# Kernel tuning notes

Hardware: AMD Instinct MI355X
Metric: run time of the kernel (lower is better)

The kernel has to match this reference:

```python
import jax, jax.numpy as jnp
import numpy as np

N_NODES = 20000   # N
N_EDGES = 320000  # E (avg degree 16)
T_STEPS = 16      # T
IN_FEATS = 1      # F
HG = 64           # hidden_g
HT = 128          # hidden_t
LN_EPS = 1e-5


def _layer_norm(x, g, b):
    mu = jnp.mean(x, axis=-1, keepdims=True)
    var = jnp.mean((x - mu) ** 2, axis=-1, keepdims=True)
    return (x - mu) * jax.lax.rsqrt(var + LN_EPS) * g + b


def setup_inputs() -> dict:
    key = jax.random.key(0)
    k = jax.random.split(key, 16)
    r = lambda i, shape, s: jax.random.normal(k[i], shape, jnp.float32) * s
    return dict(
        x_seq=jax.random.normal(k[0], (1, T_STEPS, N_NODES, IN_FEATS), jnp.float32),
        edge_index=jax.random.randint(k[1], (2, N_EDGES), 0, N_NODES, dtype=jnp.int32),
        # SAGEConv layer 0: lin_l (aggregated neighbors, has bias) + lin_r (root)
        W_l0=r(2, (IN_FEATS, HG), 0.5), W_r0=r(3, (IN_FEATS, HG), 0.5), b0=jnp.zeros((HG,), jnp.float32),
        ln0_g=jnp.ones((HG,), jnp.float32), ln0_b=jnp.zeros((HG,), jnp.float32),
        # SAGEConv layer 1
        W_l1=r(4, (HG, HG), 0.1), W_r1=r(5, (HG, HG), 0.1), b1=jnp.zeros((HG,), jnp.float32),
        ln1_g=jnp.ones((HG,), jnp.float32), ln1_b=jnp.zeros((HG,), jnp.float32),
        # GRU (torch layout: gates r,z,n stacked along first dim)
        gru_Wih=r(6, (3 * HT, HG), 0.05), gru_Whh=r(7, (3 * HT, HT), 0.05),
        gru_bih=jnp.zeros((3 * HT,), jnp.float32), gru_bhh=jnp.zeros((3 * HT,), jnp.float32),
        # head
        head_W=r(8, (HT, 1), 0.05), head_b=jnp.zeros((1,), jnp.float32),
    )


def reference(x_seq, edge_index, W_l0, W_r0, b0, ln0_g, ln0_b,
              W_l1, W_r1, b1, ln1_g, ln1_b,
              gru_Wih, gru_Whh, gru_bih, gru_bhh, head_W, head_b):
    src, dst = edge_index[0], edge_index[1]
    # in-degree for mean aggregation (clamped to 1, like PyG mean aggr on isolated nodes)
    deg = jnp.clip(jax.ops.segment_sum(jnp.ones((N_EDGES,), jnp.float32), dst,
                                       num_segments=N_NODES), 1.0)[:, None]

    def sage(x, Wl, Wr, b):
        # mean over incoming neighbors, then lin_l(aggr) + lin_r(root)
        agg = jax.ops.segment_sum(x[src], dst, num_segments=N_NODES) / deg
        return agg @ Wl + x @ Wr + b

    def stack(xt):  # xt: (N, F) -> (N, HG); dropout is identity in eval mode
        h = jax.nn.relu(_layer_norm(sage(xt, W_l0, W_r0, b0), ln0_g, ln0_b))
        h = jax.nn.relu(_layer_norm(sage(h, W_l1, W_r1, b1), ln1_g, ln1_b))
        return h

    X = x_seq[0]  # (T, N, F), B == 1
    # scan over timesteps (matches the per-t Python loop, bounds peak memory)
    _, H = jax.lax.scan(lambda c, xt: (c, stack(xt)), None, X)  # H: (T, N, HG)

    def gru_step(h, xt):  # torch GRU cell; batch = N nodes
        gi = xt @ gru_Wih.T + gru_bih
        gh = h @ gru_Whh.T + gru_bhh
        ir, iz, inn = jnp.split(gi, 3, axis=-1)
        hr, hz, hn = jnp.split(gh, 3, axis=-1)
        r = jax.nn.sigmoid(ir + hr)
        z = jax.nn.sigmoid(iz + hz)
        n = jnp.tanh(inn + r * hn)
        return (1.0 - z) * n + z * h, None

    h0 = jnp.zeros((N_NODES, HT), x_seq.dtype)
    hT, _ = jax.lax.scan(gru_step, h0, H)
    y = (hT @ head_W + head_b)[:, 0]  # (N,)
    return y
```

## Files before the change

kernel.cpp:

```cpp
#include <hip/hip_runtime.h>
#include <math.h>

#define NN 20000
#define NE 320000
#define TS 16
#define HG 64
#define HTT 128
#define NG 384
#define LN_EPS 1e-5f
#define ASTR 1032

typedef __attribute__((ext_vector_type(8))) _Float16 f16x8;
typedef __attribute__((ext_vector_type(4))) float f32x4;

__device__ __forceinline__ float wave_sum64(float v) {
  #pragma unroll
  for (int off = 32; off > 0; off >>= 1) v += __shfl_xor(v, off, 64);
  return v;
}
__device__ __forceinline__ float quad_sum16(float v) {
  #pragma unroll
  for (int off = 1; off < 16; off <<= 1) v += __shfl_xor(v, off, 64);
  return v;
}
__device__ __forceinline__ float fast_sigmoid(float x) {
  return __builtin_amdgcn_rcpf(1.f + __expf(-x));
}
__device__ __forceinline__ float fast_tanh(float x) {
  float e = __expf(-2.f * fabsf(x));
  float th = (1.f - e) * __builtin_amdgcn_rcpf(1.f + e);
  return copysignf(th, x);
}

__global__ __launch_bounds__(256) void k_setup(
    const float* __restrict__ x_seq, float* __restrict__ xT,
    const float* __restrict__ Wih, _Float16* __restrict__ WihF,
    const float* __restrict__ Whh, _Float16* __restrict__ WhhF,
    const float* __restrict__ Wl1, const float* __restrict__ Wr1,
    _Float16* __restrict__ Wchi, _Float16* __restrict__ Wclo,
    const float* __restrict__ Wl0, const float* __restrict__ Wr0,
    const float* __restrict__ b0, const float* __restrict__ g0,
    const float* __restrict__ be0, float* __restrict__ P,
    int* __restrict__ cnt) {
  int gid = blockIdx.x * 256 + threadIdx.x;
  int stride = gridDim.x * 256;
  for (int i = gid; i < NN * TS; i += stride) {
    int t = i / NN, n = i - t * NN;
    xT[n * 16 + t] = x_seq[i];
  }
  for (int i = gid; i < NG * HG; i += stride) WihF[i] = (_Float16)Wih[i];
  for (int i = gid; i < NG * HTT; i += stride) WhhF[i] = (_Float16)Whh[i];
  for (int i = gid; i < HG * 128; i += stride) {
    int n = i >> 7, k = i & 127;
    float x = (k < HG) ? Wl1[k * HG + n] : Wr1[(k - HG) * HG + n];
    _Float16 h = (_Float16)x;
    Wchi[i] = h;
    Wclo[i] = (_Float16)(x - (float)h);
  }
  for (int i = gid; i < NN; i += stride) cnt[i] = 0;
  if (blockIdx.x == 0 && threadIdx.x < 64) {
    int f = threadIdx.x;
    float u = Wl0[f], v = Wr0[f], c = b0[f], g = g0[f];
    float um = wave_sum64(u) * (1.f / 64.f);
    float vm = wave_sum64(v) * (1.f / 64.f);
    float cm = wave_sum64(c) * (1.f / 64.f);
    float uc = u - um, vc = v - vm, cc = c - cm;
    float muu = wave_sum64(uc * uc) * (1.f / 64.f);
    float mvv = wave_sum64(vc * vc) * (1.f / 64.f);
    float mcc = wave_sum64(cc * cc) * (1.f / 64.f);
    float muv = wave_sum64(uc * vc) * (1.f / 64.f);
    float muc = wave_sum64(uc * cc) * (1.f / 64.f);
    float mvc = wave_sum64(vc * cc) * (1.f / 64.f);
    P[f] = uc * g; P[64 + f] = vc * g; P[128 + f] = cc * g; P[192 + f] = be0[f];
    if (f == 0) {
      P[256] = muu; P[257] = mvv; P[258] = mcc;
      P[259] = muv; P[260] = muc; P[261] = mvc;
    }
  }
}

__global__ void k_hist(const int* __restrict__ dst, int* cnt) {
  int e = blockIdx.x * blockDim.x + threadIdx.x;
  if (e < NE) atomicAdd(&cnt[dst[e]], 1);
}

__global__ void k_scan(int* cnt, int* row_ptr, float* deg_inv) {
  __shared__ int s[1024];
  const int PER = 20;
  int tid = threadIdx.x;
  int base = tid * PER;
  int vloc[PER], dloc[PER];
  int sum = 0;
  #pragma unroll
  for (int j = 0; j < PER; j++) {
    int n = base + j;
    int d = (n < NN) ? cnt[n] : 0;
    vloc[j] = sum;
    dloc[j] = d;
    sum += d;
  }
  s[tid] = sum;
  __syncthreads();
  for (int off = 1; off < 1024; off <<= 1) {
    int t = (tid >= off) ? s[tid - off] : 0;
    __syncthreads();
    s[tid] += t;
    __syncthreads();
  }
  int excl = s[tid] - sum;
  #pragma unroll
  for (int j = 0; j < PER; j++) {
    int n = base + j;
    if (n < NN) {
      int rp = excl + vloc[j];
      row_ptr[n] = rp;
      cnt[n] = rp;
      int d = dloc[j];
      deg_inv[n] = 1.0f / (float)((d > 1) ? d : 1);
    }
  }
  if (tid == 1023) row_ptr[NN] = s[1023];
}

__global__ void k_fill(const int* __restrict__ src, const int* __restrict__ dst,
                       int* cursor, int* col) {
  int e = blockIdx.x * blockDim.x + threadIdx.x;
  if (e < NE) {
    int p = atomicAdd(&cursor[dst[e]], 1);
    col[p] = src[e];
  }
}

__global__ __launch_bounds__(256) void k_h0_fused(
    const float* __restrict__ xT,
    const int* __restrict__ row_ptr, const int* __restrict__ col,
    const float* __restrict__ deg_inv,
    const float* __restrict__ P,
    _Float16* __restrict__ h0r) {
  int lane = threadIdx.x & 63;
  int n = blockIdx.x * 4 + (threadIdx.x >> 6);
  int grp = lane >> 4, tl = lane & 15;
  int beg = row_ptr[n];
  int deg = row_ptr[n + 1] - beg;
  float s0 = 0.f, s1 = 0.f;
  int iters = (deg + 7) >> 3;
  for (int it = 0; it < iters; it++) {
    int e0 = it * 8 + grp, e1 = it * 8 + 4 + grp;
    bool v0 = e0 < deg, v1 = e1 < deg;
    int i0 = v0 ? e0 : 0, i1 = v1 ? e1 : 0;
    int c0 = col[beg + i0];
    int c1 = col[beg + i1];
    float x0 = xT[c0 * 16 + tl];
    float x1 = xT[c1 * 16 + tl];
    s0 += v0 ? x0 : 0.f;
    s1 += v1 ? x1 : 0.f;
  }
  float s = s0 + s1;
  s += __shfl_xor(s, 16, 64);
  s += __shfl_xor(s, 32, 64);
  float aggv = s * deg_inv[n];
  float xv = xT[n * 16 + tl];
  float muu = P[256], mvv = P[257], mcc = P[258];
  float muv = P[259], muc = P[260], mvc = P[261];
  #pragma unroll
  for (int half = 0; half < 2; half++) {
    int c = lane + half * 64;
    int t = c >> 3, f8 = (c & 7) * 8;
    float a = __shfl(aggv, t, 64);
    float x = __shfl(xv, t, 64);
    float var = a * a * muu + x * x * mvv + mcc
              + 2.f * (a * x * muv + a * muc + x * mvc);
    float rstd = rsqrtf(var + LN_EPS);
    f16x8 o;
    #pragma unroll
    for (int j = 0; j < 8; j++) {
      int f = f8 + j;
      float d = a * P[f] + x * P[64 + f] + P[128 + f];
      o[j] = (_Float16)fmaxf(d * rstd + P[192 + f], 0.f);
    }
    *(f16x8*)&h0r[(size_t)n * 1024 + c * 8] = o;
  }
}

__global__ __launch_bounds__(256) void k_sage_fused(
    const _Float16* __restrict__ h0r,
    const int* __restrict__ row_ptr, const int* __restrict__ col,
    const float* __restrict__ deg_inv,
    const _Float16* __restrict__ Wchi, const _Float16* __restrict__ Wclo,
    const float* __restrict__ b1, const float* __restrict__ g1, const float* __restrict__ be1,
    _Float16* __restrict__ Ht_all) {
  __shared__ _Float16 aggL[16 * ASTR];
  int tid = threadIdx.x;
  int lane = tid & 63, wave = tid >> 6;
  int col16 = lane & 15, quad = lane >> 4;
  int m0 = blockIdx.x * 16;

  for (int i = 0; i < 4; i++) {
    int nl = wave * 4 + i;
    int n = m0 + nl;
    int beg = row_ptr[n];
    int deg = row_ptr[n + 1] - beg;
    const f16x8 z = {0,0,0,0,0,0,0,0};
    f16x8 aH0 = z, aH1 = z, aH2 = z, aH3 = z;
    f16x8 aL0 = z, aL1 = z, aL2 = z, aL3 = z;
    int e = 0;
    for (; e + 8 <= deg; e += 8) {
      int c0 = col[beg + e + 0], c1 = col[beg + e + 1];
      int c2 = col[beg + e + 2], c3 = col[beg + e + 3];
      int c4 = col[beg + e + 4], c5 = col[beg + e + 5];
      int c6 = col[beg + e + 6], c7 = col[beg + e + 7];
      const f16x8* p0 = (const f16x8*)(h0r + (size_t)c0 * 1024);
      const f16x8* p1 = (const f16x8*)(h0r + (size_t)c1 * 1024);
      const f16x8* p2 = (const f16x8*)(h0r + (size_t)c2 * 1024);
      const f16x8* p3 = (const f16x8*)(h0r + (size_t)c3 * 1024);
      const f16x8* p4 = (const f16x8*)(h0r + (size_t)c4 * 1024);
      const f16x8* p5 = (const f16x8*)(h0r + (size_t)c5 * 1024);
      const f16x8* p6 = (const f16x8*)(h0r + (size_t)c6 * 1024);
      const f16x8* p7 = (const f16x8*)(h0r + (size_t)c7 * 1024);
      f16x8 d0a = p0[lane], d0b = p0[lane + 64];
      f16x8 d1a = p1[lane], d1b = p1[lane + 64];
      f16x8 d2a = p2[lane], d2b = p2[lane + 64];
      f16x8 d3a = p3[lane], d3b = p3[lane + 64];
      f16x8 d4a = p4[lane], d4b = p4[lane + 64];
      f16x8 d5a = p5[lane], d5b = p5[lane + 64];
      f16x8 d6a = p6[lane], d6b = p6[lane + 64];
      f16x8 d7a = p7[lane], d7b = p7[lane + 64];
      aH0 += d0a; aL0 += d0b;
      aH1 += d1a; aL1 += d1b;
      aH2 += d2a; aL2 += d2b;
      aH3 += d3a; aL3 += d3b;
      aH0 += d4a; aL0 += d4b;
      aH1 += d5a; aL1 += d5b;
      aH2 += d6a; aL2 += d6b;
      aH3 += d7a; aL3 += d7b;
    }
    for (; e + 4 <= deg; e += 4) {
      int c0 = col[beg + e + 0], c1 = col[beg + e + 1];
      int c2 = col[beg + e + 2], c3 = col[beg + e + 3];
      const f16x8* p0 = (const f16x8*)(h0r + (size_t)c0 * 1024);
      const f16x8* p1 = (const f16x8*)(h0r + (size_t)c1 * 1024);
      const f16x8* p2 = (const f16x8*)(h0r + (size_t)c2 * 1024);
      const f16x8* p3 = (const f16x8*)(h0r + (size_t)c3 * 1024);
      f16x8 d0a = p0[lane], d0b = p0[lane + 64];
      f16x8 d1a = p1[lane], d1b = p1[lane + 64];
      f16x8 d2a = p2[lane], d2b = p2[lane + 64];
      f16x8 d3a = p3[lane], d3b = p3[lane + 64];
      aH0 += d0a; aL0 += d0b;
      aH1 += d1a; aL1 += d1b;
      aH2 += d2a; aL2 += d2b;
      aH3 += d3a; aL3 += d3b;
    }
    for (; e < deg; e++) {
      int c = col[beg + e];
      const f16x8* p = (const f16x8*)(h0r + (size_t)c * 1024);
      aH0 += p[lane]; aL0 += p[lane + 64];
    }
    float di = deg_inv[n];
    f16x8 o0, o1;
    #pragma unroll
    for (int j = 0; j < 8; j++) {
      o0[j] = (_Float16)((((float)aH0[j] + (float)aH1[j]) +
                          ((float)aH2[j] + (float)aH3[j])) * di);
      o1[j] = (_Float16)((((float)aL0[j] + (float)aL1[j]) +
                          ((float)aL2[j] + (float)aL3[j])) * di);
    }
    *(f16x8*)&aggL[nl * ASTR + lane * 8] = o0;
    *(f16x8*)&aggL[nl * ASTR + 512 + lane * 8] = o1;
  }
  __syncthreads();

  for (int ts = 0; ts < 4; ts++) {
    int t = wave * 4 + ts;
    f32x4 acc[4];
    #pragma unroll
    for (int nt = 0; nt < 4; nt++) acc[nt] = (f32x4){0.f, 0.f, 0.f, 0.f};

    #pragma unroll
    for (int kk = 0; kk < 2; kk++) {
      f16x8 ah = *(const f16x8*)&aggL[col16 * ASTR + t * 64 + kk * 32 + quad * 8];
      #pragma unroll
      for (int nt = 0; nt < 4; nt++) {
        int nf = nt * 16 + col16;
        f16x8 bh = *(const f16x8*)&Wchi[nf * 128 + kk * 32 + quad * 8];
        f16x8 bl = *(const f16x8*)&Wclo[nf * 128 + kk * 32 + quad * 8];
        acc[nt] = __builtin_amdgcn_mfma_f32_16x16x32_f16(ah, bh, acc[nt], 0, 0, 0);
        acc[nt] = __builtin_amdgcn_mfma_f32_16x16x32_f16(ah, bl, acc[nt], 0, 0, 0);
      }
    }
    #pragma unroll
    for (int kk = 0; kk < 2; kk++) {
      f16x8 ah = *(const f16x8*)&h0r[(size_t)(m0 + col16) * 1024 + t * 64 + kk * 32 + quad * 8];
      #pragma unroll
      for (int nt = 0; nt < 4; nt++) {
        int nf = nt * 16 + col16;
        f16x8 bh = *(const f16x8*)&Wchi[nf * 128 + 64 + kk * 32 + quad * 8];
        f16x8 bl = *(const f16x8*)&Wclo[nf * 128 + 64 + kk * 32 + quad * 8];
        acc[nt] = __builtin_amdgcn_mfma_f32_16x16x32_f16(ah, bh, acc[nt], 0, 0, 0);
        acc[nt] = __builtin_amdgcn_mfma_f32_16x16x32_f16(ah, bl, acc[nt], 0, 0, 0);
      }
    }

    float bias[4], gg[4], bb[4];
    #pragma unroll
    for (int nt = 0; nt < 4; nt++) {
      int nf = nt * 16 + col16;
      bias[nt] = b1[nf]; gg[nt] = g1[nf]; bb[nt] = be1[nf];
    }
    #pragma unroll
    for (int r = 0; r < 4; r++) {
      float v[4];
      #pragma unroll
      for (int nt = 0; nt < 4; nt++) v[nt] = acc[nt][r] + bias[nt];
      float s = (v[0] + v[1]) + (v[2] + v[3]);
      float mu = quad_sum16(s) * (1.f / 64.f);
      float sq = 0.f;
      #pragma unroll
      for (int nt = 0; nt < 4; nt++) { v[nt] -= mu; sq += v[nt] * v[nt]; }
      float var = quad_sum16(sq) * (1.f / 64.f);
      float rstd = rsqrtf(var + LN_EPS);
      int m = m0 + quad * 4 + r;
      size_t base = ((size_t)t * NN + m) * HG;
      #pragma unroll
      for (int nt = 0; nt < 4; nt++) {
        float o = fmaxf(v[nt] * rstd * gg[nt] + bb[nt], 0.f);
        Ht_all[base + nt * 16 + col16] = (_Float16)o;
      }
    }
  }
}

__global__ __launch_bounds__(256, 2) void k_gru_all(
    const _Float16* __restrict__ Ht_all,
    const _Float16* __restrict__ WihF,
    const _Float16* __restrict__ WhhF,
    const float* __restrict__ bih, const float* __restrict__ bhh,
    const float* __restrict__ headW, const float* __restrict__ headb,
    float* __restrict__ out) {
  __shared__ _Float16 WihL[NG * 64];
  __shared__ _Float16 hL[2][32 * 128];
  __shared__ float yL[4][32];

  int tid = threadIdx.x;
  int lane = tid & 63, wave = tid >> 6;
  int col16 = lane & 15, quad = lane >> 4;
  int m0 = blockIdx.x * 32;
  int gb = 2 * wave;

  for (int i = tid; i < NG * 8; i += 256) {
    int g = i >> 3, k8 = i & 7;
    *(f16x8*)&WihL[g * 64 + ((k8 + g) & 7) * 8] = *(const f16x8*)&WihF[g * 64 + k8 * 8];
  }
  for (int i = tid; i < 2 * 32 * 128; i += 256) hL[0][i] = (_Float16)0.f;

  int gts[6];
  #pragma unroll
  for (int t6 = 0; t6 < 6; t6++)
    gts[t6] = (t6 < 2) ? (gb + t6) : (t6 < 4) ? (8 + gb + t6 - 2) : (16 + gb + t6 - 4);

  f16x8 wgh[4][6];
  #pragma unroll
  for (int kk = 0; kk < 4; kk++)
    #pragma unroll
    for (int t6 = 0; t6 < 6; t6++)
      wgh[kk][t6] = *(const f16x8*)&WhhF[(size_t)(gts[t6] * 16 + col16) * HTT + kk * 32 + quad * 8];

  int jj[2]; float bR[2], bZ[2], bNi[2], bNh[2], hw[2];
  int waddr[2][4][2];
  #pragma unroll
  for (int js = 0; js < 2; js++) {
    int j = (gb + js) * 16 + col16;
    jj[js] = j;
    bR[js]  = bih[j] + bhh[j];
    bZ[js]  = bih[HTT + j] + bhh[HTT + j];
    bNi[js] = bih[2 * HTT + j];
    bNh[js] = bhh[2 * HTT + j];
    hw[js]  = headW[j];
    #pragma unroll
    for (int mt = 0; mt < 2; mt++)
      #pragma unroll
      for (int r = 0; r < 4; r++) {
        int row = mt * 16 + quad * 4 + r;
        waddr[mt][r][js] = row * 128 + (((j >> 3) + row) & 15) * 8 + (j & 7);
      }
  }
  float hreg[2][4][2];
  #pragma unroll
  for (int mt = 0; mt < 2; mt++)
    #pragma unroll
    for (int r = 0; r < 4; r++) { hreg[mt][r][0] = 0.f; hreg[mt][r][1] = 0.f; }

  size_t aoff[2][2];
  #pragma unroll
  for (int kk = 0; kk < 2; kk++)
    #pragma unroll
    for (int mt = 0; mt < 2; mt++)
      aoff[kk][mt] = (size_t)(m0 + mt * 16 + col16) * HG + kk * 32 + quad * 8;

  __syncthreads();

  for (int t = 0; t < TS; t++) {
    const _Float16* hcur = hL[t & 1];
    _Float16* hnxt = hL[(t + 1) & 1];

    f32x4 acc[8][2];
    #pragma unroll
    for (int a = 0; a < 8; a++) {
      acc[a][0] = (f32x4){0.f, 0.f, 0.f, 0.f};
      acc[a][1] = (f32x4){0.f, 0.f, 0.f, 0.f};
    }

    const _Float16* AH = Ht_all + (size_t)t * NN * HG;
    f16x8 gah[2][2];
    #pragma unroll
    for (int kk = 0; kk < 2; kk++)
      #pragma unroll
      for (int mt = 0; mt < 2; mt++)
        gah[kk][mt] = *(const f16x8*)&AH[aoff[kk][mt]];

    #pragma unroll
    for (int kk = 0; kk < 4; kk++) {
      f16x8 ah[2];
      #pragma unroll
      for (int mt = 0; mt < 2; mt++) {
        int row = mt * 16 + col16;
        int k8 = kk * 4 + quad;
        ah[mt] = *(const f16x8*)&hcur[row * 128 + ((k8 + row) & 15) * 8];
      }
      #pragma unroll
      for (int t6 = 0; t6 < 6; t6++) {
        int ai = (t6 < 4) ? t6 : t6 + 2;
        #pragma unroll
        for (int mt = 0; mt < 2; mt++)
          acc[ai][mt] = __builtin_amdgcn_mfma_f32_16x16x32_f16(ah[mt], wgh[kk][t6], acc[ai][mt], 0, 0, 0);
      }
    }
    #pragma unroll
    for (int kk = 0; kk < 2; kk++) {
      #pragma unroll
      for (int t6 = 0; t6 < 6; t6++) {
        int g = gts[t6] * 16 + col16;
        int k8 = kk * 4 + quad;
        f16x8 b = *(const f16x8*)&WihL[g * 64 + ((k8 + g) & 7) * 8];
        #pragma unroll
        for (int mt = 0; mt < 2; mt++)
          acc[t6][mt] = __builtin_amdgcn_mfma_f32_16x16x32_f16(gah[kk][mt], b, acc[t6][mt], 0, 0, 0);
      }
    }

    #pragma unroll
    for (int mt = 0; mt < 2; mt++) {
      #pragma unroll
      for (int r = 0; r < 4; r++) {
        #pragma unroll
        for (int js = 0; js < 2; js++) {
          float R  = acc[0 + js][mt][r] + bR[js];
          float Z  = acc[2 + js][mt][r] + bZ[js];
          float Ni = acc[4 + js][mt][r] + bNi[js];
          float Nh = acc[6 + js][mt][r] + bNh[js];
          float rg = fast_sigmoid(R);
          float zg = fast_sigmoid(Z);
          float nn = fast_tanh(Ni + rg * Nh);
          float hn = nn + zg * (hreg[mt][r][js] - nn);
          hreg[mt][r][js] = hn;
          hnxt[waddr[mt][r][js]] = (_Float16)hn;
        }
      }
    }
    __syncthreads();
  }

  #pragma unroll
  for (int mt = 0; mt < 2; mt++) {
    #pragma unroll
    for (int r = 0; r < 4; r++) {
      float py = hreg[mt][r][0] * hw[0] + hreg[mt][r][1] * hw[1];
      py = quad_sum16(py);
      if (col16 == 0) yL[wave][mt * 16 + quad * 4 + r] = py;
    }
  }
  __syncthreads();
  if (tid < 32)
    out[m0 + tid] = yL[0][tid] + yL[1][tid] + yL[2][tid] + yL[3][tid] + headb[0];
}

extern "C" void kernel_launch(void* const* d_in, const int* in_sizes, int n_in,
                              void* d_out, int out_size, void* d_ws, size_t ws_size,
                              hipStream_t stream) {
  const float* x_seq = (const float*)d_in[0];
  const int*   edge  = (const int*)d_in[1];
  const float* Wl0   = (const float*)d_in[2];
  const float* Wr0   = (const float*)d_in[3];
  const float* b0    = (const float*)d_in[4];
  const float* g0    = (const float*)d_in[5];
  const float* be0   = (const float*)d_in[6];
  const float* Wl1   = (const float*)d_in[7];
  const float* Wr1   = (const float*)d_in[8];
  const float* b1    = (const float*)d_in[9];
  const float* g1    = (const float*)d_in[10];
  const float* be1   = (const float*)d_in[11];
  const float* Wih   = (const float*)d_in[12];
  const float* Whh   = (const float*)d_in[13];
  const float* bih   = (const float*)d_in[14];
  const float* bhh   = (const float*)d_in[15];
  const float* headW = (const float*)d_in[16];
  const float* headb = (const float*)d_in[17];
  float* out = (float*)d_out;

  const int* srcp = edge;
  const int* dstp = edge + NE;

  char* ws = (char*)d_ws;
  size_t off = 0;
  auto alloc = [&](size_t bytes) -> void* {
    void* p = ws + off;
    off += (bytes + 255) & ~(size_t)255;
    return p;
  };
  int*   cnt     = (int*)alloc(NN * 4);
  int*   row_ptr = (int*)alloc((NN + 1) * 4);
  int*   col     = (int*)alloc(NE * 4);
  float* deg_inv = (float*)alloc(NN * 4);
  float* xT      = (float*)alloc((size_t)NN * TS * 4);
  float* P       = (float*)alloc(512 * 4);
  _Float16* h0r  = (_Float16*)alloc((size_t)NN * 1024 * 2);
  _Float16* Ht_all = (_Float16*)alloc((size_t)TS * NN * HG * 2);
  _Float16* WihF = (_Float16*)alloc((size_t)NG * HG * 2);
  _Float16* WhhF = (_Float16*)alloc((size_t)NG * HTT * 2);
  _Float16* Wchi = (_Float16*)alloc((size_t)HG * 128 * 2);
  _Float16* Wclo = (_Float16*)alloc((size_t)HG * 128 * 2);
  (void)ws_size; (void)in_sizes; (void)n_in; (void)out_size;

  k_setup<<<1250, 256, 0, stream>>>(x_seq, xT, Wih, WihF, Whh, WhhF,
                                    Wl1, Wr1, Wchi, Wclo,
                                    Wl0, Wr0, b0, g0, be0, P, cnt);
  k_hist<<<(NE + 255) / 256, 256, 0, stream>>>(dstp, cnt);
  k_scan<<<1, 1024, 0, stream>>>(cnt, row_ptr, deg_inv);
  k_fill<<<(NE + 255) / 256, 256, 0, stream>>>(srcp, dstp, cnt, col);
  k_h0_fused<<<NN / 4, 256, 0, stream>>>(xT, row_ptr, col, deg_inv, P, h0r);
  k_sage_fused<<<NN / 16, 256, 0, stream>>>(h0r, row_ptr, col, deg_inv,
                                            Wchi, Wclo, b1, g1, be1, Ht_all);
  k_gru_all<<<NN / 32, 256, 0, stream>>>(Ht_all, WihF, WhhF, bih, bhh,
                                         headW, headb, out);
}
```

Baseline: 400.0 us.

## Batch neighbor gathers across four nodes per wave with zero-padded sentinel row

```diff
diff --git a/kernel.cpp b/kernel.cpp
--- a/kernel.cpp
+++ b/kernel.cpp
@@ -41,7 +41,7 @@
     const float* __restrict__ Wl0, const float* __restrict__ Wr0,
     const float* __restrict__ b0, const float* __restrict__ g0,
     const float* __restrict__ be0, float* __restrict__ P,
-    int* __restrict__ cnt) {
+    int* __restrict__ cnt, _Float16* __restrict__ h0r) {
   int gid = blockIdx.x * 256 + threadIdx.x;
   int stride = gridDim.x * 256;
   for (int i = gid; i < NN * TS; i += stride) {
@@ -58,6 +58,7 @@
     Wclo[i] = (_Float16)(x - (float)h);
   }
   for (int i = gid; i < NN; i += stride) cnt[i] = 0;
+  for (int i = gid; i < 1024; i += stride) h0r[(size_t)NN * 1024 + i] = (_Float16)0.f;
   if (blockIdx.x == 0 && threadIdx.x < 64) {
     int f = threadIdx.x;
     float u = Wl0[f], v = Wr0[f], c = b0[f], g = g0[f];
@@ -194,78 +195,94 @@
   int lane = tid & 63, wave = tid >> 6;
   int col16 = lane & 15, quad = lane >> 4;
   int m0 = blockIdx.x * 16;
-
-  for (int i = 0; i < 4; i++) {
-    int nl = wave * 4 + i;
-    int n = m0 + nl;
-    int beg = row_ptr[n];
-    int deg = row_ptr[n + 1] - beg;
-    const f16x8 z = {0,0,0,0,0,0,0,0};
-    f16x8 aH0 = z, aH1 = z, aH2 = z, aH3 = z;
-    f16x8 aL0 = z, aL1 = z, aL2 = z, aL3 = z;
-    int e = 0;
-    for (; e + 8 <= deg; e += 8) {
-      int c0 = col[beg + e + 0], c1 = col[beg + e + 1];
-      int c2 = col[beg + e + 2], c3 = col[beg + e + 3];
-      int c4 = col[beg + e + 4], c5 = col[beg + e + 5];
-      int c6 = col[beg + e + 6], c7 = col[beg + e + 7];
-      const f16x8* p0 = (const f16x8*)(h0r + (size_t)c0 * 1024);
-      const f16x8* p1 = (const f16x8*)(h0r + (size_t)c1 * 1024);
-      const f16x8* p2 = (const f16x8*)(h0r + (size_t)c2 * 1024);
-      const f16x8* p3 = (const f16x8*)(h0r + (size_t)c3 * 1024);
-      const f16x8* p4 = (const f16x8*)(h0r + (size_t)c4 * 1024);
-      const f16x8* p5 = (const f16x8*)(h0r + (size_t)c5 * 1024);
-      const f16x8* p6 = (const f16x8*)(h0r + (size_t)c6 * 1024);
-      const f16x8* p7 = (const f16x8*)(h0r + (size_t)c7 * 1024);
-      f16x8 d0a = p0[lane], d0b = p0[lane + 64];
-      f16x8 d1a = p1[lane], d1b = p1[lane + 64];
-      f16x8 d2a = p2[lane], d2b = p2[lane + 64];
-      f16x8 d3a = p3[lane], d3b = p3[lane + 64];
-      f16x8 d4a = p4[lane], d4b = p4[lane + 64];
-      f16x8 d5a = p5[lane], d5b = p5[lane + 64];
-      f16x8 d6a = p6[lane], d6b = p6[lane + 64];
-      f16x8 d7a = p7[lane], d7b = p7[lane + 64];
-      aH0 += d0a; aL0 += d0b;
-      aH1 += d1a; aL1 += d1b;
-      aH2 += d2a; aL2 += d2b;
-      aH3 += d3a; aL3 += d3b;
-      aH0 += d4a; aL0 += d4b;
-      aH1 += d5a; aL1 += d5b;
-      aH2 += d6a; aL2 += d6b;
-      aH3 += d7a; aL3 += d7b;
-    }
-    for (; e + 4 <= deg; e += 4) {
-      int c0 = col[beg + e + 0], c1 = col[beg + e + 1];
-      int c2 = col[beg + e + 2], c3 = col[beg + e + 3];
-      const f16x8* p0 = (const f16x8*)(h0r + (size_t)c0 * 1024);
-      const f16x8* p1 = (const f16x8*)(h0r + (size_t)c1 * 1024);
-      const f16x8* p2 = (const f16x8*)(h0r + (size_t)c2 * 1024);
-      const f16x8* p3 = (const f16x8*)(h0r + (size_t)c3 * 1024);
-      f16x8 d0a = p0[lane], d0b = p0[lane + 64];
-      f16x8 d1a = p1[lane], d1b = p1[lane + 64];
-      f16x8 d2a = p2[lane], d2b = p2[lane + 64];
-      f16x8 d3a = p3[lane], d3b = p3[lane + 64];
-      aH0 += d0a; aL0 += d0b;
-      aH1 += d1a; aL1 += d1b;
-      aH2 += d2a; aL2 += d2b;
-      aH3 += d3a; aL3 += d3b;
-    }
-    for (; e < deg; e++) {
-      int c = col[beg + e];
-      const f16x8* p = (const f16x8*)(h0r + (size_t)c * 1024);
-      aH0 += p[lane]; aL0 += p[lane + 64];
-    }
-    float di = deg_inv[n];
-    f16x8 o0, o1;
-    #pragma unroll
-    for (int j = 0; j < 8; j++) {
-      o0[j] = (_Float16)((((float)aH0[j] + (float)aH1[j]) +
-                          ((float)aH2[j] + (float)aH3[j])) * di);
-      o1[j] = (_Float16)((((float)aL0[j] + (float)aL1[j]) +
-                          ((float)aL2[j] + (float)aL3[j])) * di);
-    }
-    *(f16x8*)&aggL[nl * ASTR + lane * 8] = o0;
-    *(f16x8*)&aggL[nl * ASTR + 512 + lane * 8] = o1;
+  (void)deg_inv;
+
+  {
+    int i4 = lane >> 4;
+    int slot = lane & 15;
+    int ni = m0 + wave * 4 + i4;
+    int beg_i = row_ptr[ni];
+    int d_i = row_ptr[ni + 1] - beg_i;
+    int cv0 = (slot < d_i) ? col[beg_i + slot] : NN;
+    int cv1 = (slot + 16 < d_i) ? col[beg_i + 16 + slot] : NN;
+
+    int dL[4], bgL[4];
+    #pragma unroll
+    for (int i = 0; i < 4; i++) {
+      dL[i] = __builtin_amdgcn_readlane(d_i, i << 4);
+      bgL[i] = __builtin_amdgcn_readlane(beg_i, i << 4);
+    }
+    int dmax = dL[0];
+    #pragma unroll
+    for (int i = 1; i < 4; i++) if (dL[i] > dmax) dmax = dL[i];
+
+    const f16x8 z = {0, 0, 0, 0, 0, 0, 0, 0};
+    f16x8 aH[4] = {z, z, z, z}, aLo[4] = {z, z, z, z};
+
+    int emax1 = (dmax < 16) ? dmax : 16;
+    for (int e = 0; e < emax1; e += 2) {
+      f16x8 tA[4], tB[4], tC[4], tD[4];
+      #pragma unroll
+      for (int i = 0; i < 4; i++) {
+        int c0 = __builtin_amdgcn_readlane(cv0, (i << 4) | e);
+        int c1 = __builtin_amdgcn_readlane(cv0, (i << 4) | (e + 1));
+        const f16x8* p0 = (const f16x8*)(h0r + (size_t)c0 * 1024);
+        const f16x8* p1 = (const f16x8*)(h0r + (size_t)c1 * 1024);
+        tA[i] = p0[lane]; tB[i] = p0[lane + 64];
+        tC[i] = p1[lane]; tD[i] = p1[lane + 64];
+      }
+      #pragma unroll
+      for (int i = 0; i < 4; i++) {
+        aH[i]  += tA[i] + tC[i];
+        aLo[i] += tB[i] + tD[i];
+      }
+    }
+    if (dmax > 16) {
+      int emax2 = (dmax < 32) ? dmax : 32;
+      for (int e = 16; e < emax2; e += 2) {
+        f16x8 tA[4], tB[4], tC[4], tD[4];
+        #pragma unroll
+        for (int i = 0; i < 4; i++) {
+          int c0 = __builtin_amdgcn_readlane(cv1, (i << 4) | (e - 16));
+          int c1 = __builtin_amdgcn_readlane(cv1, (i << 4) | (e - 15));
+          const f16x8* p0 = (const f16x8*)(h0r + (size_t)c0 * 1024);
+          const f16x8* p1 = (const f16x8*)(h0r + (size_t)c1 * 1024);
+          tA[i] = p0[lane]; tB[i] = p0[lane + 64];
+          tC[i] = p1[lane]; tD[i] = p1[lane + 64];
+        }
+        #pragma unroll
+        for (int i = 0; i < 4; i++) {
+          aH[i]  += tA[i] + tC[i];
+          aLo[i] += tB[i] + tD[i];
+        }
+      }
+      if (dmax > 32) {
+        #pragma unroll
+        for (int i = 0; i < 4; i++) {
+          for (int e = 32; e < dL[i]; e++) {
+            int c = col[bgL[i] + e];
+            const f16x8* p = (const f16x8*)(h0r + (size_t)c * 1024);
+            aH[i]  += p[lane];
+            aLo[i] += p[lane + 64];
+          }
+        }
+      }
+    }
+
+    #pragma unroll
+    for (int i = 0; i < 4; i++) {
+      int dd = dL[i];
+      float di = 1.0f / (float)((dd > 1) ? dd : 1);
+      f16x8 o0, o1;
+      #pragma unroll
+      for (int j = 0; j < 8; j++) {
+        o0[j] = (_Float16)((float)aH[i][j] * di);
+        o1[j] = (_Float16)((float)aLo[i][j] * di);
+      }
+      int nl = wave * 4 + i;
+      *(f16x8*)&aggL[nl * ASTR + lane * 8] = o0;
+      *(f16x8*)&aggL[nl * ASTR + 512 + lane * 8] = o1;
+    }
   }
   __syncthreads();
 
@@ -522,7 +539,7 @@
   float* deg_inv = (float*)alloc(NN * 4);
   float* xT      = (float*)alloc((size_t)NN * TS * 4);
   float* P       = (float*)alloc(512 * 4);
-  _Float16* h0r  = (_Float16*)alloc((size_t)NN * 1024 * 2);
+  _Float16* h0r  = (_Float16*)alloc((size_t)(NN + 1) * 1024 * 2);
   _Float16* Ht_all = (_Float16*)alloc((size_t)TS * NN * HG * 2);
   _Float16* WihF = (_Float16*)alloc((size_t)NG * HG * 2);
   _Float16* WhhF = (_Float16*)alloc((size_t)NG * HTT * 2);
@@ -532,7 +549,7 @@
 
   k_setup<<<1250, 256, 0, stream>>>(x_seq, xT, Wih, WihF, Whh, WhhF,
                                     Wl1, Wr1, Wchi, Wclo,
-                                    Wl0, Wr0, b0, g0, be0, P, cnt);
+                                    Wl0, Wr0, b0, g0, be0, P, cnt, h0r);
   k_hist<<<(NE + 255) / 256, 256, 0, stream>>>(dstp, cnt);
   k_scan<<<1, 1024, 0, stream>>>(cnt, row_ptr, deg_inv);
   k_fill<<<(NE + 255) / 256, 256, 0, stream>>>(srcp, dstp, cnt, col);
```

Result: faster. 390.3 us (-2.4%).
